# Optimization experiments

Measured on AMD Instinct MI355X. Metric: run time of the kernel, lower is better.

## Reference

```python
import jax, jax.numpy as jnp
import numpy as np

B, N_FEAT, D = 16384, 32, 64
HID1, HID2, HOF = 1024, 512, 64
OUT = 1
N_PAIRS = N_FEAT * (N_FEAT - 1) // 2
EPS = 1e-5


def setup_inputs() -> dict:
    key = jax.random.key(0)
    ks = jax.random.split(key, 16)
    s = 0.02
    return {
        "x": jax.random.normal(ks[0], (B, N_FEAT, D), dtype=jnp.float32),
        "W1": jax.random.normal(ks[1], (N_FEAT * D, HID1), dtype=jnp.float32) * s,
        "b1": jnp.zeros((HID1,), jnp.float32),
        "g1": jnp.ones((HID1,), jnp.float32),
        "beta1": jnp.zeros((HID1,), jnp.float32),
        "W2": jax.random.normal(ks[2], (HID1, HID2), dtype=jnp.float32) * s,
        "b2": jnp.zeros((HID2,), jnp.float32),
        "g2": jnp.ones((HID2,), jnp.float32),
        "beta2": jnp.zeros((HID2,), jnp.float32),
        "W3": jax.random.normal(ks[3], (HID2, HOF), dtype=jnp.float32) * s,
        "b3": jnp.zeros((HOF,), jnp.float32),
        "Wc": jax.random.normal(ks[4], (HOF + N_PAIRS, OUT), dtype=jnp.float32) * s,
        "bc": jnp.zeros((OUT,), jnp.float32),
    }


def _batchnorm(h, g, beta):
    # BatchNorm1d in training mode: batch mean / biased variance
    m = jnp.mean(h, axis=0)
    v = jnp.var(h, axis=0)
    return g * (h - m) * jax.lax.rsqrt(v + EPS) + beta


_IU, _JU = np.triu_indices(N_FEAT, k=1)  # same (i<j) order as nested loop


def reference(x, W1, b1, g1, beta1, W2, b2, g2, beta2, W3, b3, Wc, bc):
    # second-order interactions: all pairwise dot products, gathered upper-tri
    gram = jnp.einsum("bnd,bmd->bnm", x, x)          # [B, N, N]
    pairs = gram[:, _IU, _JU]                          # [B, N*(N-1)/2]
    # deep processor
    flat = x.reshape(x.shape[0], -1)                   # [B, N*D]
    h = _batchnorm(jax.nn.relu(flat @ W1 + b1), g1, beta1)
    h = _batchnorm(jax.nn.relu(h @ W2 + b2), g2, beta2)
    hof = h @ W3 + b3                                  # [B, HOF]
    inter = jnp.concatenate([hof, pairs], axis=1)
    return inter @ Wc + bc
```

## Files before the change

### kernel.cpp

```cpp
#include <hip/hip_runtime.h>
#include <stdint.h>

typedef unsigned short u16;
typedef unsigned char u8;
typedef __attribute__((ext_vector_type(8))) short short8;
typedef __attribute__((ext_vector_type(4))) float f32x4;
typedef __attribute__((ext_vector_type(16))) float f32x16;
typedef __attribute__((ext_vector_type(4))) int i32x4;
typedef __attribute__((ext_vector_type(8))) int i32x8;

#define BATCH 16384L
#define WSCALE 64.0f
#define INV_WSCALE (1.0f / 64.0f)
#define SCALE_ONE 0x7f7f7f7f
#define INVB (1.0f / 16384.0f)

__device__ __forceinline__ u16 f2bf_trunc(float f) {
    union { float f; uint32_t u; } cv; cv.f = f;
    return (u16)(cv.u >> 16);
}
__device__ __forceinline__ float bf2f(u16 h) {
    union { uint32_t u; float f; } cv; cv.u = ((uint32_t)h) << 16;
    return cv.f;
}
template<bool HI>
__device__ __forceinline__ uint32_t fp8pk(float a, float b, uint32_t old) {
    return (uint32_t)__builtin_amdgcn_cvt_pk_fp8_f32(a, b, (int)old, HI);
}
__device__ __forceinline__ u8 f2fp8(float v) {
    return (u8)(__builtin_amdgcn_cvt_pk_fp8_f32(v, v, 0, false) & 0xff);
}

__global__ __launch_bounds__(256) void k_gram(const float* __restrict__ x,
                                              const float* __restrict__ Wc,
                                              u8* __restrict__ xb,
                                              float* __restrict__ spair,
                                              float* __restrict__ stats) {
    if (blockIdx.x == 0) {
        for (int j = threadIdx.x; j < 3072; j += 256) stats[j] = 0.f;
    }
    const int wave = threadIdx.x >> 6;
    const int lane = threadIdx.x & 63;
    const long b = (long)blockIdx.x * 4 + wave;
    const int r16 = lane & 15, quad = lane >> 4;
    const float* xg = x + b * 2048;

    short8 hi[2][2], lo[2][2];
    for (int mt = 0; mt < 2; mt++) {
        for (int k0 = 0; k0 < 2; k0++) {
            const int row = mt * 16 + r16;
            const int kof = k0 * 32 + quad * 8;
            const float* p = xg + row * 64 + kof;
            float4 p0 = *(const float4*)p;
            float4 p1 = *(const float4*)(p + 4);
            float v[8] = {p0.x, p0.y, p0.z, p0.w, p1.x, p1.y, p1.z, p1.w};
            short8 h, l;
            for (int j = 0; j < 8; j++) {
                u16 hb = f2bf_trunc(v[j]);
                h[j] = (short)hb;
                l[j] = (short)f2bf_trunc(v[j] - bf2f(hb));
            }
            hi[mt][k0] = h; lo[mt][k0] = l;
            uint32_t w0 = fp8pk<false>(v[0], v[1], 0); w0 = fp8pk<true>(v[2], v[3], w0);
            uint32_t w1 = fp8pk<false>(v[4], v[5], 0); w1 = fp8pk<true>(v[6], v[7], w1);
            *(uint2*)(xb + b * 2048 + row * 64 + kof) = make_uint2(w0, w1);
        }
    }
    f32x4 zero = {0.f, 0.f, 0.f, 0.f};
    f32x4 acc[2][2];
    for (int mt = 0; mt < 2; mt++) for (int nt = 0; nt < 2; nt++) acc[mt][nt] = zero;
    for (int k0 = 0; k0 < 2; k0++)
        for (int mt = 0; mt < 2; mt++)
            for (int nt = 0; nt < 2; nt++) {
                acc[mt][nt] = __builtin_amdgcn_mfma_f32_16x16x32_bf16(hi[mt][k0], hi[nt][k0], acc[mt][nt], 0, 0, 0);
                acc[mt][nt] = __builtin_amdgcn_mfma_f32_16x16x32_bf16(hi[mt][k0], lo[nt][k0], acc[mt][nt], 0, 0, 0);
                acc[mt][nt] = __builtin_amdgcn_mfma_f32_16x16x32_bf16(lo[mt][k0], hi[nt][k0], acc[mt][nt], 0, 0, 0);
            }
    float pacc = 0.f;
    for (int mt = 0; mt < 2; mt++)
        for (int nt = 0; nt < 2; nt++)
            for (int r = 0; r < 4; r++) {
                int row = mt * 16 + quad * 4 + r;
                int col = nt * 16 + r16;
                if (col > row) {
                    int p = 31 * row - (row * (row - 1)) / 2 + (col - row - 1);
                    pacc += acc[mt][nt][r] * Wc[64 + p];
                }
            }
    for (int off = 1; off < 64; off <<= 1) pacc += __shfl_xor(pacc, off);
    if (lane == 0) spair[b] = pacc;
}

__global__ __launch_bounds__(256) void k_transpose_fp8(const float* __restrict__ W,
                                                       u8* __restrict__ WT,
                                                       int K, int N) {
    __shared__ float tile[32][33];
    const int nb = blockIdx.x * 32, kb = blockIdx.y * 32;
    const int tx = threadIdx.x & 31, ty = threadIdx.x >> 5;
    for (int r = ty; r < 32; r += 8)
        tile[r][tx] = W[(long)(kb + r) * N + nb + tx];
    __syncthreads();
    for (int r = ty; r < 32; r += 8)
        WT[(long)(nb + r) * K + kb + tx] = f2fp8(WSCALE * tile[tx][r]);
}

__device__ __forceinline__ i32x8 frag32(const u8* __restrict__ lds, int R, int cb) {
    const int s = R & 7;
    i32x4 lo = *(const i32x4*)&lds[R * 128 + ((cb ^ s) * 16)];
    i32x4 hi = *(const i32x4*)&lds[R * 128 + (((cb + 1) ^ s) * 16)];
    i32x8 r;
    r[0] = lo[0]; r[1] = lo[1]; r[2] = lo[2]; r[3] = lo[3];
    r[4] = hi[0]; r[5] = hi[1]; r[6] = hi[2]; r[7] = hi[3];
    return r;
}

template<int LOGNB>
__global__ __launch_bounds__(256) void gemm_bn(const u8* __restrict__ A,
                                               const u8* __restrict__ Bt,
                                               const float* __restrict__ bias,
                                               u8* __restrict__ C,
                                               float* __restrict__ sums,
                                               float* __restrict__ ssq,
                                               int N, int K, float inv) {
    __shared__ u8 lA[128 * 128];
    __shared__ u8 lB[128 * 128];
    const int tid = threadIdx.x;
    const int lane = tid & 63, wave = tid >> 6;
    const int wm = wave >> 1, wn = wave & 1;
    const int r32 = lane & 31, hf = lane >> 5;
    const int lid = blockIdx.x;
    const int xcd = lid & 7, t = lid >> 3;
    const int nbk = t & ((1 << LOGNB) - 1);
    const int mbk = (xcd << 4) + (t >> LOGNB);
    const long m0 = (long)mbk * 128;
    const long n0 = (long)nbk * 128;

    f32x16 acc[2][2];
    for (int mt = 0; mt < 2; mt++)
        for (int nt = 0; nt < 2; nt++)
            for (int r = 0; r < 16; r++) acc[mt][nt][r] = 0.f;

    for (long k0 = 0; k0 < K; k0 += 128) {
        __syncthreads();
        for (int i = 0; i < 4; i++) {
            const int c = tid + 256 * i;
            const int row = c >> 3, pos = c & 7;
            const int g = pos ^ (row & 7);
            const u8* ga = A + (m0 + row) * K + k0 + g * 16;
            const u8* gb = Bt + (n0 + row) * K + k0 + g * 16;
            __builtin_amdgcn_global_load_lds((const __attribute__((address_space(1))) void*)ga,
                                             (__attribute__((address_space(3))) void*)(&lA[c * 16]), 16, 0, 0);
            __builtin_amdgcn_global_load_lds((const __attribute__((address_space(1))) void*)gb,
                                             (__attribute__((address_space(3))) void*)(&lB[c * 16]), 16, 0, 0);
        }
        __syncthreads();
        for (int km = 0; km < 2; km++) {
            const int cb = km * 4 + hf * 2;
            i32x8 af[2], bfr[2];
            for (int mt = 0; mt < 2; mt++)
                af[mt] = frag32(lA, wm * 64 + mt * 32 + r32, cb);
            for (int nt = 0; nt < 2; nt++)
                bfr[nt] = frag32(lB, wn * 64 + nt * 32 + r32, cb);
            for (int mt = 0; mt < 2; mt++)
                for (int nt = 0; nt < 2; nt++)
                    acc[mt][nt] = __builtin_amdgcn_mfma_scale_f32_32x32x64_f8f6f4(
                        af[mt], bfr[nt], acc[mt][nt], 0, 0,
                        0, SCALE_ONE, 0, SCALE_ONE);
        }
    }

    for (int nt = 0; nt < 2; nt++) {
        const int col = (int)n0 + wn * 64 + nt * 32 + r32;
        const float bcol = bias[col];
        float s = 0.f, sq = 0.f;
        for (int mt = 0; mt < 2; mt++)
            for (int r = 0; r < 16; r++) {
                const long row = m0 + wm * 64 + mt * 32 + 4 * hf + (r & 3) + 8 * (r >> 2);
                float v = acc[mt][nt][r] * inv + bcol;
                v = fmaxf(v, 0.f);
                C[row * N + col] = f2fp8(v);
                s += v; sq += v * v;
            }
        s += __shfl_xor(s, 32);
        sq += __shfl_xor(sq, 32);
        if (hf == 0) { atomicAdd(&sums[col], s); atomicAdd(&ssq[col], sq); }
    }
}

__global__ __launch_bounds__(256) void k_mid(const float* __restrict__ sums1,
                                             const float* __restrict__ ssq1,
                                             const float* __restrict__ g1,
                                             const float* __restrict__ beta1,
                                             const float* __restrict__ W2,
                                             const float* __restrict__ b2,
                                             u8* __restrict__ w2f,
                                             float* __restrict__ b2a) {
    const int bid = blockIdx.x;
    if (bid < 512) {
        __shared__ float tile[32][33];
        __shared__ float sc[32];
        const int nb = (bid & 15) * 32;
        const int kb = (bid >> 4) * 32;
        const int tx = threadIdx.x & 31, ty = threadIdx.x >> 5;
        if (threadIdx.x < 32) {
            const int k = kb + threadIdx.x;
            const float m = sums1[k] * INVB;
            const float var = ssq1[k] * INVB - m * m;
            sc[threadIdx.x] = g1[k] * rsqrtf(var + 1e-5f);
        }
        __syncthreads();
        for (int r = ty; r < 32; r += 8)
            tile[r][tx] = sc[r] * W2[(long)(kb + r) * 512 + nb + tx];
        __syncthreads();
        for (int r = ty; r < 32; r += 8)
            w2f[(long)(nb + r) * 1024 + kb + tx] = f2fp8(WSCALE * tile[tx][r]);
    } else {
        __shared__ float c1s[1024];
        __shared__ float part[4][64];
        for (int k = threadIdx.x; k < 1024; k += 256) {
            const float m = sums1[k] * INVB;
            const float var = ssq1[k] * INVB - m * m;
            const float a = g1[k] * rsqrtf(var + 1e-5f);
            c1s[k] = beta1[k] - a * m;
        }
        __syncthreads();
        const int lane = threadIdx.x & 63, w = threadIdx.x >> 6;
        const int col = (bid - 512) * 64 + lane;
        float s = 0.f;
        for (int k = w * 256; k < w * 256 + 256; k++)
            s += c1s[k] * W2[(long)k * 512 + col];
        part[w][lane] = s;
        __syncthreads();
        if (w == 0)
            b2a[col] = b2[col] + part[0][lane] + part[1][lane] + part[2][lane] + part[3][lane];
    }
}

__global__ void k_stat2v(const float* __restrict__ sums, const float* __restrict__ ssq,
                         const float* __restrict__ g, const float* __restrict__ beta,
                         float* __restrict__ a, float* __restrict__ c, float invB,
                         const float* __restrict__ W3, const float* __restrict__ b3,
                         const float* __restrict__ Wc, const float* __restrict__ bc,
                         float* __restrict__ v, float* __restrict__ c0) {
    if (blockIdx.x < 2) {
        const int k = blockIdx.x * 256 + threadIdx.x;
        const float m = sums[k] * invB;
        const float var = ssq[k] * invB - m * m;
        const float s = g[k] * rsqrtf(var + 1e-5f);
        a[k] = s; c[k] = beta[k] - s * m;
    } else {
        for (int k = threadIdx.x; k < 512; k += 256) {
            float s = 0.f;
            for (int j = 0; j < 64; j++) s += W3[k * 64 + j] * Wc[j];
            v[k] = s;
        }
        if (threadIdx.x == 0) {
            float s = 0.f;
            for (int j = 0; j < 64; j++) s += b3[j] * Wc[j];
            *c0 = s + bc[0];
        }
    }
}

__global__ __launch_bounds__(256) void k_final(const u8* __restrict__ h2,
                                               const float* __restrict__ a2,
                                               const float* __restrict__ c2,
                                               const float* __restrict__ v,
                                               const float* __restrict__ c0,
                                               const float* __restrict__ spair,
                                               float* __restrict__ out) {
    const int wave = threadIdx.x >> 6, lane = threadIdx.x & 63;
    const long b = (long)blockIdx.x * 4 + wave;
    const int k0 = lane * 8;
    uint2 hv = *(const uint2*)&h2[b * 512 + k0];
    float f[8];
    f[0] = __builtin_amdgcn_cvt_f32_fp8(hv.x, 0);
    f[1] = __builtin_amdgcn_cvt_f32_fp8(hv.x, 1);
    f[2] = __builtin_amdgcn_cvt_f32_fp8(hv.x, 2);
    f[3] = __builtin_amdgcn_cvt_f32_fp8(hv.x, 3);
    f[4] = __builtin_amdgcn_cvt_f32_fp8(hv.y, 0);
    f[5] = __builtin_amdgcn_cvt_f32_fp8(hv.y, 1);
    f[6] = __builtin_amdgcn_cvt_f32_fp8(hv.y, 2);
    f[7] = __builtin_amdgcn_cvt_f32_fp8(hv.y, 3);
    float acc = 0.f;
    for (int j = 0; j < 8; j++) {
        const int k = k0 + j;
        acc += (a2[k] * f[j] + c2[k]) * v[k];
    }
    for (int off = 1; off < 64; off <<= 1) acc += __shfl_xor(acc, off);
    if (lane == 0) out[b] = acc + spair[b] + c0[0];
}

extern "C" void kernel_launch(void* const* d_in, const int* in_sizes, int n_in,
                              void* d_out, int out_size, void* d_ws, size_t ws_size,
                              hipStream_t stream) {
    const float* x     = (const float*)d_in[0];
    const float* W1    = (const float*)d_in[1];
    const float* b1    = (const float*)d_in[2];
    const float* g1    = (const float*)d_in[3];
    const float* beta1 = (const float*)d_in[4];
    const float* W2    = (const float*)d_in[5];
    const float* b2    = (const float*)d_in[6];
    const float* g2    = (const float*)d_in[7];
    const float* beta2 = (const float*)d_in[8];
    const float* W3    = (const float*)d_in[9];
    const float* b3    = (const float*)d_in[10];
    const float* Wc    = (const float*)d_in[11];
    const float* bc    = (const float*)d_in[12];
    float* out = (float*)d_out;

    char* ws = (char*)d_ws;
    size_t o = 0;
    u8* xb  = (u8*)(ws + o); o += BATCH * 2048;
    u8* w1f = (u8*)(ws + o); o += 2048L * 1024;
    u8* w2f = (u8*)(ws + o); o += 1024L * 512;
    u8* h1b = (u8*)(ws + o); o += BATCH * 1024;
    u8* h2b = (u8*)(ws + o); o += BATCH * 512;
    float* spair = (float*)(ws + o); o += BATCH * 4;
    float* stats = (float*)(ws + o); o += 3072 * 4;
    float* sums1 = stats, *ssq1 = stats + 1024, *sums2 = stats + 2048, *ssq2 = stats + 2560;
    float* a2 = (float*)(ws + o); o += 512 * 4;
    float* c2 = (float*)(ws + o); o += 512 * 4;
    float* vv = (float*)(ws + o); o += 512 * 4;
    float* c0 = (float*)(ws + o); o += 4;
    float* b2a = (float*)(ws + o); o += 512 * 4;

    k_gram<<<4096, 256, 0, stream>>>(x, Wc, xb, spair, stats);
    k_transpose_fp8<<<dim3(1024 / 32, 2048 / 32), 256, 0, stream>>>(W1, w1f, 2048, 1024);
    gemm_bn<3><<<1024, 256, 0, stream>>>(xb, w1f, b1, h1b, sums1, ssq1, 1024, 2048, INV_WSCALE);
    k_mid<<<520, 256, 0, stream>>>(sums1, ssq1, g1, beta1, W2, b2, w2f, b2a);
    gemm_bn<2><<<512, 256, 0, stream>>>(h1b, w2f, b2a, h2b, sums2, ssq2, 512, 1024, INV_WSCALE);
    k_stat2v<<<3, 256, 0, stream>>>(sums2, ssq2, g2, beta2, a2, c2, INVB,
                                    W3, b3, Wc, bc, vv, c0);
    k_final<<<4096, 256, 0, stream>>>(h2b, a2, c2, vv, c0, spair, out);
}
```

Measured before the change: 308.5 us.

## Use 256x256 double-buffered FP8 GEMM for layer 1 and fuse W1 transpose into gram

```diff
diff --git a/kernel.cpp b/kernel.cpp
--- a/kernel.cpp
+++ b/kernel.cpp
@@ -33,9 +33,24 @@
 
 __global__ __launch_bounds__(256) void k_gram(const float* __restrict__ x,
                                               const float* __restrict__ Wc,
+                                              const float* __restrict__ W1,
                                               u8* __restrict__ xb,
+                                              u8* __restrict__ w1f,
                                               float* __restrict__ spair,
                                               float* __restrict__ stats) {
+    if (blockIdx.x >= 4096) {
+        __shared__ float tile[32][33];
+        const int bid2 = blockIdx.x - 4096;
+        const int nb = (bid2 & 31) * 32;
+        const int kb = (bid2 >> 5) * 32;
+        const int tx = threadIdx.x & 31, ty = threadIdx.x >> 5;
+        for (int r = ty; r < 32; r += 8)
+            tile[r][tx] = W1[(long)(kb + r) * 1024 + nb + tx];
+        __syncthreads();
+        for (int r = ty; r < 32; r += 8)
+            w1f[(long)(nb + r) * 2048 + kb + tx] = f2fp8(WSCALE * tile[tx][r]);
+        return;
+    }
     if (blockIdx.x == 0) {
         for (int j = threadIdx.x; j < 3072; j += 256) stats[j] = 0.f;
     }
@@ -91,19 +106,6 @@
     if (lane == 0) spair[b] = pacc;
 }
 
-__global__ __launch_bounds__(256) void k_transpose_fp8(const float* __restrict__ W,
-                                                       u8* __restrict__ WT,
-                                                       int K, int N) {
-    __shared__ float tile[32][33];
-    const int nb = blockIdx.x * 32, kb = blockIdx.y * 32;
-    const int tx = threadIdx.x & 31, ty = threadIdx.x >> 5;
-    for (int r = ty; r < 32; r += 8)
-        tile[r][tx] = W[(long)(kb + r) * N + nb + tx];
-    __syncthreads();
-    for (int r = ty; r < 32; r += 8)
-        WT[(long)(nb + r) * K + kb + tx] = f2fp8(WSCALE * tile[tx][r]);
-}
-
 __device__ __forceinline__ i32x8 frag32(const u8* __restrict__ lds, int R, int cb) {
     const int s = R & 7;
     i32x4 lo = *(const i32x4*)&lds[R * 128 + ((cb ^ s) * 16)];
@@ -112,6 +114,154 @@
     r[0] = lo[0]; r[1] = lo[1]; r[2] = lo[2]; r[3] = lo[3];
     r[4] = hi[0]; r[5] = hi[1]; r[6] = hi[2]; r[7] = hi[3];
     return r;
+}
+
+template<int LOGNB>
+__global__ __launch_bounds__(512) void gemm_bn8(const u8* __restrict__ A,
+                                                const u8* __restrict__ Bt,
+                                                const float* __restrict__ bias,
+                                                u8* __restrict__ C,
+                                                float* __restrict__ sums,
+                                                float* __restrict__ ssq,
+                                                int N, int K, float inv) {
+    __shared__ u8 lA[2][32768];
+    __shared__ u8 lB[2][32768];
+    const int tid = threadIdx.x;
+    const int lane = tid & 63, wave = tid >> 6;
+    const int wm = wave >> 2, wn = wave & 3;
+    const int r32 = lane & 31, hf = lane >> 5;
+    const int lid = blockIdx.x;
+    const int xcd = lid & 7, t = lid >> 3;
+    const int nbk = t & ((1 << LOGNB) - 1);
+    const int mbk = xcd * (32 >> LOGNB) + (t >> LOGNB);
+    const long m0 = (long)mbk * 256;
+    const long n0 = (long)nbk * 256;
+
+    const u8* srcA[4]; const u8* srcB[4]; int dstc[4];
+#pragma unroll
+    for (int i = 0; i < 4; i++) {
+        const int c = tid + 512 * i;
+        const int row = c >> 3, pos = c & 7;
+        const int g = pos ^ (row & 7);
+        srcA[i] = A + (m0 + row) * (long)K + g * 16;
+        srcB[i] = Bt + (n0 + row) * (long)K + g * 16;
+        dstc[i] = c * 16;
+    }
+
+    f32x16 acc[4][2];
+#pragma unroll
+    for (int mt = 0; mt < 4; mt++)
+#pragma unroll
+        for (int nt = 0; nt < 2; nt++)
+#pragma unroll
+            for (int r = 0; r < 16; r++) acc[mt][nt][r] = 0.f;
+
+#pragma unroll
+    for (int i = 0; i < 4; i++)
+        __builtin_amdgcn_global_load_lds((const __attribute__((address_space(1))) void*)srcA[i],
+                                         (__attribute__((address_space(3))) void*)(&lA[0][dstc[i]]), 16, 0, 0);
+#pragma unroll
+    for (int i = 0; i < 4; i++)
+        __builtin_amdgcn_global_load_lds((const __attribute__((address_space(1))) void*)srcB[i],
+                                         (__attribute__((address_space(3))) void*)(&lB[0][dstc[i]]), 16, 0, 0);
+    __syncthreads();
+
+    const int NT = K >> 7;
+    for (int ti = 0; ti < NT; ti++) {
+        const int cur = ti & 1, nxt = cur ^ 1;
+        const long koff = (long)(ti + 1) << 7;
+        const bool pf = (ti + 1 < NT);
+        const u8* la = &lA[cur][0];
+        const u8* lb = &lB[cur][0];
+        i32x8 af[4], bf;
+
+#pragma unroll
+        for (int mt = 0; mt < 4; mt++)
+            af[mt] = frag32(la, wm * 128 + mt * 32 + r32, hf * 2);
+        bf = frag32(lb, wn * 64 + r32, hf * 2);
+        if (pf) {
+#pragma unroll
+            for (int i = 0; i < 4; i++)
+                __builtin_amdgcn_global_load_lds((const __attribute__((address_space(1))) void*)(srcA[i] + koff),
+                                                 (__attribute__((address_space(3))) void*)(&lA[nxt][dstc[i]]), 16, 0, 0);
+        }
+        __builtin_amdgcn_s_barrier();
+        asm volatile("s_waitcnt lgkmcnt(0)" ::: "memory");
+        __builtin_amdgcn_sched_barrier(0);
+        __builtin_amdgcn_s_setprio(1);
+#pragma unroll
+        for (int mt = 0; mt < 4; mt++)
+            acc[mt][0] = __builtin_amdgcn_mfma_scale_f32_32x32x64_f8f6f4(
+                af[mt], bf, acc[mt][0], 0, 0, 0, SCALE_ONE, 0, SCALE_ONE);
+        __builtin_amdgcn_s_setprio(0);
+        __builtin_amdgcn_s_barrier();
+
+        bf = frag32(lb, wn * 64 + 32 + r32, hf * 2);
+        if (pf) {
+#pragma unroll
+            for (int i = 0; i < 4; i++)
+                __builtin_amdgcn_global_load_lds((const __attribute__((address_space(1))) void*)(srcB[i] + koff),
+                                                 (__attribute__((address_space(3))) void*)(&lB[nxt][dstc[i]]), 16, 0, 0);
+        }
+        __builtin_amdgcn_s_barrier();
+        asm volatile("s_waitcnt lgkmcnt(0)" ::: "memory");
+        __builtin_amdgcn_sched_barrier(0);
+        __builtin_amdgcn_s_setprio(1);
+#pragma unroll
+        for (int mt = 0; mt < 4; mt++)
+            acc[mt][1] = __builtin_amdgcn_mfma_scale_f32_32x32x64_f8f6f4(
+                af[mt], bf, acc[mt][1], 0, 0, 0, SCALE_ONE, 0, SCALE_ONE);
+        __builtin_amdgcn_s_setprio(0);
+        __builtin_amdgcn_s_barrier();
+
+#pragma unroll
+        for (int mt = 0; mt < 4; mt++)
+            af[mt] = frag32(la, wm * 128 + mt * 32 + r32, 4 + hf * 2);
+        bf = frag32(lb, wn * 64 + r32, 4 + hf * 2);
+        __builtin_amdgcn_s_barrier();
+        asm volatile("s_waitcnt lgkmcnt(0)" ::: "memory");
+        __builtin_amdgcn_sched_barrier(0);
+        __builtin_amdgcn_s_setprio(1);
+#pragma unroll
+        for (int mt = 0; mt < 4; mt++)
+            acc[mt][0] = __builtin_amdgcn_mfma_scale_f32_32x32x64_f8f6f4(
+                af[mt], bf, acc[mt][0], 0, 0, 0, SCALE_ONE, 0, SCALE_ONE);
+        __builtin_amdgcn_s_setprio(0);
+        __builtin_amdgcn_s_barrier();
+
+        bf = frag32(lb, wn * 64 + 32 + r32, 4 + hf * 2);
+        __builtin_amdgcn_s_barrier();
+        asm volatile("s_waitcnt lgkmcnt(0)" ::: "memory");
+        __builtin_amdgcn_sched_barrier(0);
+        __builtin_amdgcn_s_setprio(1);
+#pragma unroll
+        for (int mt = 0; mt < 4; mt++)
+            acc[mt][1] = __builtin_amdgcn_mfma_scale_f32_32x32x64_f8f6f4(
+                af[mt], bf, acc[mt][1], 0, 0, 0, SCALE_ONE, 0, SCALE_ONE);
+        __builtin_amdgcn_s_setprio(0);
+        asm volatile("s_waitcnt vmcnt(0)" ::: "memory");
+        __builtin_amdgcn_s_barrier();
+    }
+
+#pragma unroll
+    for (int nt = 0; nt < 2; nt++) {
+        const int col = (int)n0 + wn * 64 + nt * 32 + r32;
+        const float bcol = bias[col];
+        float s = 0.f, sq = 0.f;
+#pragma unroll
+        for (int mt = 0; mt < 4; mt++)
+#pragma unroll
+            for (int r = 0; r < 16; r++) {
+                const long row = m0 + wm * 128 + mt * 32 + 4 * hf + (r & 3) + 8 * (r >> 2);
+                float v = acc[mt][nt][r] * inv + bcol;
+                v = fmaxf(v, 0.f);
+                C[row * N + col] = f2fp8(v);
+                s += v; sq += v * v;
+            }
+        s += __shfl_xor(s, 32);
+        sq += __shfl_xor(sq, 32);
+        if (hf == 0) { atomicAdd(&sums[col], s); atomicAdd(&ssq[col], sq); }
+    }
 }
 
 template<int LOGNB>
@@ -325,9 +475,8 @@
     float* c0 = (float*)(ws + o); o += 4;
     float* b2a = (float*)(ws + o); o += 512 * 4;
 
-    k_gram<<<4096, 256, 0, stream>>>(x, Wc, xb, spair, stats);
-    k_transpose_fp8<<<dim3(1024 / 32, 2048 / 32), 256, 0, stream>>>(W1, w1f, 2048, 1024);
-    gemm_bn<3><<<1024, 256, 0, stream>>>(xb, w1f, b1, h1b, sums1, ssq1, 1024, 2048, INV_WSCALE);
+    k_gram<<<6144, 256, 0, stream>>>(x, Wc, W1, xb, w1f, spair, stats);
+    gemm_bn8<2><<<256, 512, 0, stream>>>(xb, w1f, b1, h1b, sums1, ssq1, 1024, 2048, INV_WSCALE);
     k_mid<<<520, 256, 0, stream>>>(sums1, ssq1, g1, beta1, W2, b2, w2f, b2a);
     gemm_bn<2><<<512, 256, 0, stream>>>(h1b, w2f, b2a, h2b, sums2, ssq2, 512, 1024, INV_WSCALE);
     k_stat2v<<<3, 256, 0, stream>>>(sums2, ssq2, g2, beta2, a2, c2, INVB,
```

After: 305.5 us. No clear change (-1.0%).
